# Kernel optimization log

Hardware: AMD Instinct MI355X
Metric: run time of the kernel (lower is better)

The kernel has to match this reference:

```python
import jax, jax.numpy as jnp
import numpy as np

B, T, H, S = 4, 4096, 32, 64   # batch, seq_len, n_head, head_size (n_embd = H*S = 2048)
SCALE = 1.0 / 128.0            # matches wkv(..., scale=1/128) in time_mixing_v5_1


def setup_inputs() -> dict:
    key = jax.random.key(0)
    ks = jax.random.split(key, 5)
    k = jax.random.normal(ks[0], (B, T, H, S), dtype=jnp.float32)
    v = jax.random.normal(ks[1], (B, T, H, S), dtype=jnp.float32)
    r = jax.random.normal(ks[2], (B, T, H, S), dtype=jnp.float32)
    state2 = jnp.zeros((B, H, S, S), dtype=jnp.float32)
    # time_first = exp(w) > 0 in the original; time_decay = exp(-exp(w)) in (0,1)
    time_first = jax.random.uniform(ks[3], (H, S, 1), dtype=jnp.float32, minval=0.1, maxval=1.0)
    time_decay = jax.random.uniform(ks[4], (H, S, 1), dtype=jnp.float32, minval=0.9, maxval=0.999)
    return {"k": k, "v": v, "r": r, "state2": state2,
            "time_first": time_first, "time_decay": time_decay}


def reference(k, v, r, state2, time_first, time_decay):
    """RWKV-5 WKV recurrence (wkv() applied token-by-token via lax.scan).

    Per step (per head):
        s2    = state2 * SCALE
        kv    = k_t (outer) (v_t * SCALE)            # [H,S,S]
        wkv_t = r_t @ (time_first * kv + s2)         # [H,S]
        state2' = (time_decay * s2 + kv) / SCALE
    """
    def scan_one(s0, k_b, v_b, r_b):
        def step(s_raw, inp):
            k_t, v_t, r_t = inp                       # each [H, S]
            s2 = s_raw * SCALE
            kv = jnp.einsum('hs,hd->hsd', k_t, v_t * SCALE)   # outer product per head
            wkv = jnp.einsum('hs,hsd->hd', r_t, time_first * kv + s2)
            s_new = (time_decay * s2 + kv) / SCALE
            return s_new, wkv
        s_final, out = jax.lax.scan(step, s0, (k_b, v_b, r_b))
        return out, s_final                           # out: [T, H, S]

    out, s_final = jax.vmap(scan_one)(state2, k, v, r)
    return out, s_final
```

## Files before the change

kernel.cpp:

```cpp
#include <hip/hip_runtime.h>


namespace {
constexpr int cB = 4, cT = 4096, cH = 32, cS = 64;
constexpr int cTS = cH * cS;
constexpr float cScale = 1.0f / 128.0f;
constexpr int cSC = 8, cSCL = cT / cSC;
constexpr int cL = 64, cNS = cSCL / cL;
constexpr int cBH = cB * cH;
}

typedef float  v2f   __attribute__((ext_vector_type(2)));
typedef __bf16 bf16x8 __attribute__((ext_vector_type(8)));
typedef float  f32x16 __attribute__((ext_vector_type(16)));
typedef unsigned short u16x4 __attribute__((ext_vector_type(4)));
typedef unsigned short u16x8 __attribute__((ext_vector_type(8)));
typedef unsigned int   u32x2 __attribute__((ext_vector_type(2)));
typedef unsigned int   u32x4 __attribute__((ext_vector_type(4)));

#define BARRIER() asm volatile("s_waitcnt lgkmcnt(0)\n\ts_barrier" ::: "memory")

__device__ __forceinline__ float hw_log2(float x) { return __builtin_amdgcn_logf(x); }
__device__ __forceinline__ float hw_exp2(float x) { return __builtin_amdgcn_exp2f(x); }

__device__ __forceinline__ int swzb(int row, int byteInRow) {
    return row * 128 + (byteInRow ^ ((row & 15) << 3));
}
__device__ __forceinline__ int swzbV(int row, int byteInRow) {
    return row * 128 + (byteInRow ^ ((row & 15) << 3) ^ (((row >> 3) & 7) << 4));
}
__device__ __forceinline__ int crow(int r, int hi) {
    return (r & 3) + 8 * (r >> 2) + 4 * hi;
}
__device__ __forceinline__ unsigned short bfb(float x) {
    return __builtin_bit_cast(unsigned short, (__bf16)x);
}
__device__ __forceinline__ bf16x8 ldRowFrag(const unsigned short* T, int row, int col) {
    const char* p = (const char*)T;
    u16x4 a = *(const u16x4*)(p + swzb(row, col * 2));
    u16x4 b = *(const u16x4*)(p + swzb(row, col * 2 + 8));
    u16x8 r = {a[0], a[1], a[2], a[3], b[0], b[1], b[2], b[3]};
    return __builtin_bit_cast(bf16x8, r);
}
__device__ __forceinline__ bf16x8 ldRowFragV(const unsigned short* T, int row, int col) {
    const char* p = (const char*)T;
    u16x4 a = *(const u16x4*)(p + swzbV(row, col * 2));
    u16x4 b = *(const u16x4*)(p + swzbV(row, col * 2 + 8));
    u16x8 r = {a[0], a[1], a[2], a[3], b[0], b[1], b[2], b[3]};
    return __builtin_bit_cast(bf16x8, r);
}
__device__ __forceinline__ bf16x8 ldColFrag(const unsigned short* T, int row0, int col) {
    const char* p = (const char*)T;
    u16x8 r;
#pragma unroll
    for (int e = 0; e < 8; ++e)
        r[e] = *(const unsigned short*)(p + swzb(row0 + e, col * 2));
    return __builtin_bit_cast(bf16x8, r);
}
__device__ __forceinline__ void stRow8(unsigned short* T, int row, int col, u16x8 v) {
    char* p = (char*)T;
    u16x4 a = {v[0], v[1], v[2], v[3]}, b = {v[4], v[5], v[6], v[7]};
    *(u16x4*)(p + swzb(row, col * 2)) = a;
    *(u16x4*)(p + swzb(row, col * 2 + 8)) = b;
}
__device__ __forceinline__ void stElV16(unsigned short* T, int row, int col,
                                        unsigned short v) {
    *(unsigned short*)((char*)T + swzbV(row, col * 2)) = v;
}
__device__ __forceinline__ unsigned cvtpk(float a, float b) {
    unsigned r;
    asm("v_cvt_pk_bf16_f32 %0, %1, %2" : "=v"(r) : "v"(a), "v"(b));
    return r;
}
__device__ __forceinline__ void pack2(const f32x16& m, bf16x8& f0, bf16x8& f1) {
#pragma unroll
    for (int g2 = 0; g2 < 2; ++g2) {
        const int bs = 8 * g2;
        unsigned A0 = cvtpk(m[bs + 0], m[bs + 1]);
        unsigned A1 = cvtpk(m[bs + 2], m[bs + 3]);
        unsigned B0 = cvtpk(m[bs + 4], m[bs + 5]);
        unsigned B1 = cvtpk(m[bs + 6], m[bs + 7]);
        u32x2 r0 = __builtin_amdgcn_permlane32_swap(A0, B0, false, false);
        u32x2 r1 = __builtin_amdgcn_permlane32_swap(A1, B1, false, false);
        u32x4 w = {r0[0], r1[0], r0[1], r1[1]};
        if (g2 == 0) f0 = __builtin_bit_cast(bf16x8, w);
        else         f1 = __builtin_bit_cast(bf16x8, w);
    }
}

__global__ __launch_bounds__(256)
void rwkv5_pass1(const float* __restrict__ K, const float* __restrict__ V,
                 const float* __restrict__ TD, float* __restrict__ Buf) {
    __shared__ alignas(16) unsigned short KWs[2][4096], VSTs[2][4096];
    const int bh = blockIdx.x, sc = blockIdx.y;
    const int b = bh >> 5, h = bh & 31;
    const int tid = threadIdx.x, wid = tid >> 6, l = tid & 63;
    const int lo = l & 31, hi = l >> 5;
    const int dhs = wid >> 1, shs = wid & 1;
    const int dS = lo + 32 * dhs, sS = lo + 32 * shs;
    const size_t tbase = ((size_t)b * cT + (size_t)sc * cSCL) * cTS + h * cS;
    const float *kb = K + tbase, *vb = V + tbase;

    const int st = tid >> 2, c16 = (tid & 3) * 16;
    float ipw[16];
#pragma unroll
    for (int e = 0; e < 16; ++e) {
        const float l2 = hw_log2(TD[h * cS + c16 + e]);
        ipw[e] = hw_exp2(-(float)(st + 1) * l2);
    }
    float tdL = TD[h * cS + sS];
#pragma unroll
    for (int i = 0; i < 6; ++i) tdL *= tdL;

    float kx[16], vx[16];
    auto gload = [&](int cc) {
        const size_t off = ((size_t)(cc * cL + st)) * cTS + c16;
#pragma unroll
        for (int i = 0; i < 4; ++i) {
            *(float4*)&kx[i * 4] = *(const float4*)(kb + off + i * 4);
            *(float4*)&vx[i * 4] = *(const float4*)(vb + off + i * 4);
        }
    };
    auto tileWrite = [&](int bi) {
        const v2f* kx2  = (const v2f*)kx;
        const v2f* vx2  = (const v2f*)vx;
        const v2f* ipw2 = (const v2f*)ipw;
        u16x8 w;
#pragma unroll
        for (int hf = 0; hf < 2; ++hf) {
#pragma unroll
            for (int e2 = 0; e2 < 4; ++e2) {
                v2f m = kx2[hf * 4 + e2] * ipw2[hf * 4 + e2];
                w[2 * e2]     = bfb(m.x);
                w[2 * e2 + 1] = bfb(m.y);
            }
            stRow8(KWs[bi], st, c16 + hf * 8, w);
        }
        const v2f sc2 = {cScale, cScale};
#pragma unroll
        for (int e2 = 0; e2 < 8; ++e2) {
            v2f m = vx2[e2] * sc2;
            stElV16(VSTs[bi], c16 + 2 * e2,     st, bfb(m.x));
            stElV16(VSTs[bi], c16 + 2 * e2 + 1, st, bfb(m.y));
        }
    };

    f32x16 x;
#pragma unroll
    for (int i = 0; i < 16; ++i) x[i] = 0.f;

    gload(0); tileWrite(0); gload(1);
    BARRIER();
#pragma unroll 1
    for (int c = 0; c < cNS; ++c) {
        const int cur = c & 1, nxt = cur ^ 1;
        f32x16 w;
#pragma unroll
        for (int i = 0; i < 16; ++i) w[i] = 0.f;
        __builtin_amdgcn_s_setprio(1);
#pragma unroll
        for (int ks = 0; ks < 4; ++ks) {
            bf16x8 vaf = ldRowFragV(VSTs[cur], dS, ks * 16 + hi * 8);
            bf16x8 kcf = ldColFrag(KWs[cur], ks * 16 + hi * 8, sS);
            w = __builtin_amdgcn_mfma_f32_32x32x16_bf16(vaf, kcf, w, 0, 0, 0);
        }
        __builtin_amdgcn_s_setprio(0);
#pragma unroll
        for (int i = 0; i < 16; ++i) x[i] = tdL * (x[i] + w[i]);
        if (c + 1 < cNS) tileWrite(nxt);
        if (c + 2 < cNS) gload(c + 2);
        BARRIER();
    }
    float* xp = Buf + ((size_t)bh * cSC + sc) * cS * cS;
#pragma unroll
    for (int r = 0; r < 16; ++r)
        xp[(size_t)sS * cS + crow(r, hi) + 32 * dhs] = x[r];
}

__global__ __launch_bounds__(256)
void rwkv5_pass2(const float* __restrict__ S2in, const float* __restrict__ TD,
                 float* __restrict__ Buf) {
    const int bh = blockIdx.x, h = bh & 31;
    const int t = threadIdx.x, s = t >> 2, db = (t & 3) * 16;
    float d = TD[h * cS + s];
#pragma unroll
    for (int i = 0; i < 9; ++i) d *= d;
    float4 x[4];
    const float* s0 = S2in + ((size_t)bh * cS + s) * cS + db;
#pragma unroll
    for (int i = 0; i < 4; ++i) {
        x[i] = *(const float4*)(s0 + i * 4);
        x[i].x *= cScale; x[i].y *= cScale; x[i].z *= cScale; x[i].w *= cScale;
    }
    for (int sc = 0; sc < cSC; ++sc) {
        float* base = Buf + (((size_t)bh * cSC + sc) * cS + s) * cS + db;
        float4 pr[4];
        if (sc < cSC - 1) {
#pragma unroll
            for (int i = 0; i < 4; ++i) pr[i] = *(const float4*)(base + i * 4);
        }
#pragma unroll
        for (int i = 0; i < 4; ++i) *(float4*)(base + i * 4) = x[i];
        if (sc < cSC - 1) {
#pragma unroll
            for (int i = 0; i < 4; ++i) {
                x[i].x = fmaf(d, x[i].x, pr[i].x);
                x[i].y = fmaf(d, x[i].y, pr[i].y);
                x[i].z = fmaf(d, x[i].z, pr[i].z);
                x[i].w = fmaf(d, x[i].w, pr[i].w);
            }
        }
    }
}

__global__ __launch_bounds__(512)
void rwkv5_pass3(const float* __restrict__ K, const float* __restrict__ V,
                 const float* __restrict__ R, const float* __restrict__ TF,
                 const float* __restrict__ TD, const float* __restrict__ Buf,
                 float* __restrict__ Out) {
    __shared__ alignas(16) unsigned short RWs[2][4096], KWs[2][4096],
                                          VSTs[2][4096];
    __shared__ alignas(16) u32x4 XTF[2][2][4][64];
    __shared__ float DIAGs[2][64];
    const int u = blockIdx.x, bh = u >> 3, sc = u & 7;
    const int b = bh >> 5, h = bh & 31;
    const int tid = threadIdx.x, wid = tid >> 6, l = tid & 63;
    const int lo = l & 31, hi = l >> 5;
    const size_t tbase = ((size_t)b * cT + (size_t)sc * cSCL) * cTS + h * cS;
    const float *kb = K + tbase, *vb = V + tbase, *rb = R + tbase;
    float* ob = Out + tbase;

    const int st = tid >> 3, sc8 = (tid & 7) * 8;
    float pwA[8], ipwB[8], tfv[8];
#pragma unroll
    for (int e = 0; e < 8; ++e) {
        const float l2 = hw_log2(TD[h * cS + sc8 + e]);
        pwA[e]  = hw_exp2((float)st * l2);
        ipwB[e] = hw_exp2(-(float)(st + 1) * l2);
        tfv[e]  = TF[h * cS + sc8 + e];
    }
    float kx[8], vx[8], rx[8];
    auto gload = [&](int cc) {
        const size_t off = ((size_t)(cc * cL + st)) * cTS + sc8;
        *(float4*)&kx[0] = *(const float4*)(kb + off);
        *(float4*)&kx[4] = *(const float4*)(kb + off + 4);
        *(float4*)&vx[0] = *(const float4*)(vb + off);
        *(float4*)&vx[4] = *(const float4*)(vb + off + 4);
        *(float4*)&rx[0] = *(const float4*)(rb + off);
        *(float4*)&rx[4] = *(const float4*)(rb + off + 4);
    };
    auto tileWrite = [&](int bi) {
        const v2f* kx2  = (const v2f*)kx;
        const v2f* rx2  = (const v2f*)rx;
        const v2f* vx2  = (const v2f*)vx;
        const v2f* pwA2 = (const v2f*)pwA;
        const v2f* ipw2 = (const v2f*)ipwB;
        const v2f* tf2  = (const v2f*)tfv;
        u16x8 w;
#pragma unroll
        for (int e2 = 0; e2 < 4; ++e2) {
            v2f m = rx2[e2] * pwA2[e2];
            w[2 * e2]     = bfb(m.x);
            w[2 * e2 + 1] = bfb(m.y);
        }
        stRow8(RWs[bi], st, sc8, w);
#pragma unroll
        for (int e2 = 0; e2 < 4; ++e2) {
            v2f m = kx2[e2] * ipw2[e2];
            w[2 * e2]     = bfb(m.x);
            w[2 * e2 + 1] = bfb(m.y);
        }
        stRow8(KWs[bi], st, sc8, w);
        const v2f sc2 = {cScale, cScale};
#pragma unroll
        for (int e2 = 0; e2 < 4; ++e2) {
            v2f m = vx2[e2] * sc2;
            stElV16(VSTs[bi], sc8 + 2 * e2,     st, bfb(m.x));
            stElV16(VSTs[bi], sc8 + 2 * e2 + 1, st, bfb(m.y));
        }
        v2f p2 = {0.f, 0.f};
#pragma unroll
        for (int e2 = 0; e2 < 4; ++e2)
            p2 = (rx2[e2] * kx2[e2]) * tf2[e2] + p2;
        float p = p2.x + p2.y;
        p += __shfl_xor(p, 1, 64);
        p += __shfl_xor(p, 2, 64);
        p += __shfl_xor(p, 4, 64);
        if ((tid & 7) == 0) DIAGs[bi][st] = p;
    };

    const int ih = (wid >> 1) & 1, dh = wid & 1;
    const int shs = (wid >> 1) & 1, dhs = wid & 1;

    f32x16 x;
    float tdLr[16];
    if (wid >= 4) {
        const float* xin = Buf + ((size_t)bh * cSC + sc) * cS * cS;
#pragma unroll
        for (int r = 0; r < 16; ++r) {
            const int s = crow(r, hi) + 32 * shs;
            x[r] = xin[(size_t)s * cS + lo + 32 * dhs];
            float t = TD[h * cS + s];
#pragma unroll
            for (int i = 0; i < 6; ++i) t *= t;
            tdLr[r] = t;
        }
        bf16x8 f0, f1;
        pack2(x, f0, f1);
        XTF[0][dhs][2 * shs][l]     = __builtin_bit_cast(u32x4, f0);
        XTF[0][dhs][2 * shs + 1][l] = __builtin_bit_cast(u32x4, f1);
    }
    gload(0); tileWrite(0); gload(1);
    BARRIER();

#pragma unroll 1
    for (int c = 0; c < cNS; ++c) {
        const int cur = c & 1, nxt = cur ^ 1;
        if (wid < 4) {
            bf16x8 rwf[4];
#pragma unroll
            for (int ks = 0; ks < 4; ++ks)
                rwf[ks] = ldRowFrag(RWs[cur], lo + 32 * ih, ks * 16 + hi * 8);
            bf16x8 af0, af1, af2, af3;
            if (ih == 1) {
                f32x16 aU;
#pragma unroll
                for (int i = 0; i < 16; ++i) aU[i] = 0.f;
                __builtin_amdgcn_s_setprio(1);
#pragma unroll
                for (int ks = 0; ks < 4; ++ks) {
                    bf16x8 kwf = ldRowFrag(KWs[cur], lo, ks * 16 + hi * 8);
                    aU = __builtin_amdgcn_mfma_f32_32x32x16_bf16(kwf, rwf[ks], aU, 0, 0, 0);
                }
                __builtin_amdgcn_s_setprio(0);
                pack2(aU, af0, af1);
            }
            f32x16 aM;
#pragma unroll
            for (int i = 0; i < 16; ++i) aM[i] = 0.f;
            __builtin_amdgcn_s_setprio(1);
#pragma unroll
            for (int ks = 0; ks < 4; ++ks) {
                bf16x8 kwf = ldRowFrag(KWs[cur], lo + 32 * ih, ks * 16 + hi * 8);
                aM = __builtin_amdgcn_mfma_f32_32x32x16_bf16(kwf, rwf[ks], aM, 0, 0, 0);
            }
            __builtin_amdgcn_s_setprio(0);
            const float diagv = DIAGs[cur][lo + 32 * ih];
#pragma unroll
            for (int r = 0; r < 16; ++r) {
                const int cr = crow(r, hi);
                aM[r] = (lo > cr) ? aM[r] : ((lo == cr) ? diagv : 0.f);
            }
            if (ih == 1) pack2(aM, af2, af3);
            else         pack2(aM, af0, af1);
            f32x16 o;
#pragma unroll
            for (int i = 0; i < 16; ++i) o[i] = 0.f;
            __builtin_amdgcn_s_setprio(1);
            o = __builtin_amdgcn_mfma_f32_32x32x16_bf16(
                af0, ldRowFragV(VSTs[cur], lo + 32 * dh, 0 * 16 + hi * 8), o, 0, 0, 0);
            o = __builtin_amdgcn_mfma_f32_32x32x16_bf16(
                af1, ldRowFragV(VSTs[cur], lo + 32 * dh, 1 * 16 + hi * 8), o, 0, 0, 0);
            if (ih == 1) {
                o = __builtin_amdgcn_mfma_f32_32x32x16_bf16(
                    af2, ldRowFragV(VSTs[cur], lo + 32 * dh, 2 * 16 + hi * 8), o, 0, 0, 0);
                o = __builtin_amdgcn_mfma_f32_32x32x16_bf16(
                    af3, ldRowFragV(VSTs[cur], lo + 32 * dh, 3 * 16 + hi * 8), o, 0, 0, 0);
            }
#pragma unroll
            for (int ks = 0; ks < 4; ++ks) {
                bf16x8 xf = __builtin_bit_cast(bf16x8, XTF[cur][dh][ks][l]);
                o = __builtin_amdgcn_mfma_f32_32x32x16_bf16(rwf[ks], xf, o, 0, 0, 0);
            }
            __builtin_amdgcn_s_setprio(0);
            const int t0 = c * cL;
#pragma unroll
            for (int r = 0; r < 16; ++r)
                ob[(size_t)(t0 + crow(r, hi) + 32 * ih) * cTS + 32 * dh + lo] = o[r];
        } else {
            f32x16 w;
#pragma unroll
            for (int i = 0; i < 16; ++i) w[i] = 0.f;
            __builtin_amdgcn_s_setprio(1);
#pragma unroll
            for (int ks = 0; ks < 4; ++ks) {
                bf16x8 kcf = ldColFrag(KWs[cur], ks * 16 + hi * 8, lo + 32 * shs);
                bf16x8 vaf = ldRowFragV(VSTs[cur], lo + 32 * dhs, ks * 16 + hi * 8);
                w = __builtin_amdgcn_mfma_f32_32x32x16_bf16(kcf, vaf, w, 0, 0, 0);
            }
            __builtin_amdgcn_s_setprio(0);
#pragma unroll
            for (int i = 0; i < 16; ++i) x[i] = tdLr[i] * (x[i] + w[i]);
            if (c + 1 < cNS) {
                bf16x8 f0, f1;
                pack2(x, f0, f1);
                XTF[nxt][dhs][2 * shs][l]     = __builtin_bit_cast(u32x4, f0);
                XTF[nxt][dhs][2 * shs + 1][l] = __builtin_bit_cast(u32x4, f1);
            }
        }
        if (c + 1 < cNS) tileWrite(nxt);
        if (c + 2 < cNS) gload(c + 2);
        BARRIER();
    }
    if (wid >= 4 && sc == cSC - 1) {
        float* o2 = Out + (size_t)cB * cT * cTS + (size_t)bh * cS * cS;
#pragma unroll
        for (int r = 0; r < 16; ++r) {
            const int s = crow(r, hi) + 32 * shs;
            o2[(size_t)s * cS + lo + 32 * dhs] = x[r] * 128.0f;
        }
    }
}

extern "C" void kernel_launch(void* const* d_in, const int* in_sizes, int n_in,
                              void* d_out, int out_size, void* d_ws,
                              size_t ws_size, hipStream_t stream) {
    const float* K    = (const float*)d_in[0];
    const float* V    = (const float*)d_in[1];
    const float* R    = (const float*)d_in[2];
    const float* S2in = (const float*)d_in[3];
    const float* TF   = (const float*)d_in[4];
    const float* TD   = (const float*)d_in[5];
    float* OutP = (float*)d_out;
    float* Buf  = (float*)d_ws;
    (void)in_sizes; (void)n_in; (void)ws_size; (void)out_size;

    rwkv5_pass1<<<dim3(cBH, cSC - 1), dim3(256), 0, stream>>>(K, V, TD, Buf);
    rwkv5_pass2<<<dim3(cBH), dim3(256), 0, stream>>>(S2in, TD, Buf);
    rwkv5_pass3<<<dim3(cBH * cSC), dim3(512), 0, stream>>>(K, V, R, TF, TD,
                                                           Buf, OutP);
}
```

Before: 176.1 us.

## Warp-specialize pass1 producers/consumers and fold state prefix scan into pass3

Pass1 now launches 512 threads: four waves only stage K/V tiles into LDS (global load and bf16 conversion) while the other four only run the MFMA chunk-state accumulation, so loads overlap with compute. The separate pass2 kernel that prefix-scanned chunk states is removed. Each pass3 block instead rebuilds its starting state from the initial state plus the preceding chunk sums, weighted by decay^512. This saves a launch and a serialized small kernel, at the cost of redundant prefix work in later-chunk blocks (up to 7 extra 64x64 reads) and an extra S2in read in pass3.

Result: no change. 175.3 us (-0.5%).

```diff
diff --git a/kernel.cpp b/kernel.cpp
--- a/kernel.cpp
+++ b/kernel.cpp
@@ -88,7 +88,7 @@
     }
 }
 
-__global__ __launch_bounds__(256)
+__global__ __launch_bounds__(512)
 void rwkv5_pass1(const float* __restrict__ K, const float* __restrict__ V,
                  const float* __restrict__ TD, float* __restrict__ Buf) {
     __shared__ alignas(16) unsigned short KWs[2][4096], VSTs[2][4096];
@@ -96,21 +96,26 @@
     const int b = bh >> 5, h = bh & 31;
     const int tid = threadIdx.x, wid = tid >> 6, l = tid & 63;
     const int lo = l & 31, hi = l >> 5;
-    const int dhs = wid >> 1, shs = wid & 1;
+    const int dhs = (wid >> 1) & 1, shs = wid & 1;
     const int dS = lo + 32 * dhs, sS = lo + 32 * shs;
+    const int sid = tid - 256;
+    const int st = (sid & 255) >> 2, c16 = (sid & 3) * 16;
     const size_t tbase = ((size_t)b * cT + (size_t)sc * cSCL) * cTS + h * cS;
     const float *kb = K + tbase, *vb = V + tbase;
 
-    const int st = tid >> 2, c16 = (tid & 3) * 16;
     float ipw[16];
-#pragma unroll
-    for (int e = 0; e < 16; ++e) {
-        const float l2 = hw_log2(TD[h * cS + c16 + e]);
-        ipw[e] = hw_exp2(-(float)(st + 1) * l2);
-    }
-    float tdL = TD[h * cS + sS];
-#pragma unroll
-    for (int i = 0; i < 6; ++i) tdL *= tdL;
+    float tdL = 1.0f;
+    if (wid >= 4) {
+#pragma unroll
+        for (int e = 0; e < 16; ++e) {
+            const float l2 = hw_log2(TD[h * cS + c16 + e]);
+            ipw[e] = hw_exp2(-(float)(st + 1) * l2);
+        }
+    } else {
+        tdL = TD[h * cS + sS];
+#pragma unroll
+        for (int i = 0; i < 6; ++i) tdL *= tdL;
+    }
 
     float kx[16], vx[16];
     auto gload = [&](int cc) {
@@ -149,75 +154,44 @@
 #pragma unroll
     for (int i = 0; i < 16; ++i) x[i] = 0.f;
 
-    gload(0); tileWrite(0); gload(1);
+    if (wid >= 4) { gload(0); tileWrite(0); gload(1); }
     BARRIER();
 #pragma unroll 1
     for (int c = 0; c < cNS; ++c) {
         const int cur = c & 1, nxt = cur ^ 1;
-        f32x16 w;
-#pragma unroll
-        for (int i = 0; i < 16; ++i) w[i] = 0.f;
-        __builtin_amdgcn_s_setprio(1);
-#pragma unroll
-        for (int ks = 0; ks < 4; ++ks) {
-            bf16x8 vaf = ldRowFragV(VSTs[cur], dS, ks * 16 + hi * 8);
-            bf16x8 kcf = ldColFrag(KWs[cur], ks * 16 + hi * 8, sS);
-            w = __builtin_amdgcn_mfma_f32_32x32x16_bf16(vaf, kcf, w, 0, 0, 0);
-        }
-        __builtin_amdgcn_s_setprio(0);
-#pragma unroll
-        for (int i = 0; i < 16; ++i) x[i] = tdL * (x[i] + w[i]);
-        if (c + 1 < cNS) tileWrite(nxt);
-        if (c + 2 < cNS) gload(c + 2);
+        if (wid < 4) {
+            f32x16 w;
+#pragma unroll
+            for (int i = 0; i < 16; ++i) w[i] = 0.f;
+            __builtin_amdgcn_s_setprio(1);
+#pragma unroll
+            for (int ks = 0; ks < 4; ++ks) {
+                bf16x8 vaf = ldRowFragV(VSTs[cur], dS, ks * 16 + hi * 8);
+                bf16x8 kcf = ldColFrag(KWs[cur], ks * 16 + hi * 8, sS);
+                w = __builtin_amdgcn_mfma_f32_32x32x16_bf16(vaf, kcf, w, 0, 0, 0);
+            }
+            __builtin_amdgcn_s_setprio(0);
+#pragma unroll
+            for (int i = 0; i < 16; ++i) x[i] = tdL * (x[i] + w[i]);
+        } else {
+            if (c + 1 < cNS) tileWrite(nxt);
+            if (c + 2 < cNS) gload(c + 2);
+        }
         BARRIER();
     }
-    float* xp = Buf + ((size_t)bh * cSC + sc) * cS * cS;
-#pragma unroll
-    for (int r = 0; r < 16; ++r)
-        xp[(size_t)sS * cS + crow(r, hi) + 32 * dhs] = x[r];
-}
-
-__global__ __launch_bounds__(256)
-void rwkv5_pass2(const float* __restrict__ S2in, const float* __restrict__ TD,
-                 float* __restrict__ Buf) {
-    const int bh = blockIdx.x, h = bh & 31;
-    const int t = threadIdx.x, s = t >> 2, db = (t & 3) * 16;
-    float d = TD[h * cS + s];
-#pragma unroll
-    for (int i = 0; i < 9; ++i) d *= d;
-    float4 x[4];
-    const float* s0 = S2in + ((size_t)bh * cS + s) * cS + db;
-#pragma unroll
-    for (int i = 0; i < 4; ++i) {
-        x[i] = *(const float4*)(s0 + i * 4);
-        x[i].x *= cScale; x[i].y *= cScale; x[i].z *= cScale; x[i].w *= cScale;
-    }
-    for (int sc = 0; sc < cSC; ++sc) {
-        float* base = Buf + (((size_t)bh * cSC + sc) * cS + s) * cS + db;
-        float4 pr[4];
-        if (sc < cSC - 1) {
-#pragma unroll
-            for (int i = 0; i < 4; ++i) pr[i] = *(const float4*)(base + i * 4);
-        }
-#pragma unroll
-        for (int i = 0; i < 4; ++i) *(float4*)(base + i * 4) = x[i];
-        if (sc < cSC - 1) {
-#pragma unroll
-            for (int i = 0; i < 4; ++i) {
-                x[i].x = fmaf(d, x[i].x, pr[i].x);
-                x[i].y = fmaf(d, x[i].y, pr[i].y);
-                x[i].z = fmaf(d, x[i].z, pr[i].z);
-                x[i].w = fmaf(d, x[i].w, pr[i].w);
-            }
-        }
+    if (wid < 4) {
+        float* xp = Buf + ((size_t)bh * cSC + sc) * cS * cS;
+#pragma unroll
+        for (int r = 0; r < 16; ++r)
+            xp[(size_t)sS * cS + crow(r, hi) + 32 * dhs] = x[r];
     }
 }
 
 __global__ __launch_bounds__(512)
 void rwkv5_pass3(const float* __restrict__ K, const float* __restrict__ V,
-                 const float* __restrict__ R, const float* __restrict__ TF,
-                 const float* __restrict__ TD, const float* __restrict__ Buf,
-                 float* __restrict__ Out) {
+                 const float* __restrict__ R, const float* __restrict__ S2in,
+                 const float* __restrict__ TF, const float* __restrict__ TD,
+                 const float* __restrict__ Buf, float* __restrict__ Out) {
     __shared__ alignas(16) unsigned short RWs[2][4096], KWs[2][4096],
                                           VSTs[2][4096];
     __shared__ alignas(16) u32x4 XTF[2][2][4][64];
@@ -295,15 +269,27 @@
     f32x16 x;
     float tdLr[16];
     if (wid >= 4) {
-        const float* xin = Buf + ((size_t)bh * cSC + sc) * cS * cS;
+        const float* s2p = S2in + (size_t)bh * cS * cS;
+        float d512[16];
 #pragma unroll
         for (int r = 0; r < 16; ++r) {
             const int s = crow(r, hi) + 32 * shs;
-            x[r] = xin[(size_t)s * cS + lo + 32 * dhs];
             float t = TD[h * cS + s];
 #pragma unroll
             for (int i = 0; i < 6; ++i) t *= t;
             tdLr[r] = t;
+            t *= t; t *= t; t *= t;
+            d512[r] = t;
+            x[r] = s2p[(size_t)s * cS + lo + 32 * dhs] * cScale;
+        }
+#pragma unroll 1
+        for (int j = 0; j < sc; ++j) {
+            const float* pj = Buf + ((size_t)bh * cSC + j) * cS * cS;
+#pragma unroll
+            for (int r = 0; r < 16; ++r) {
+                const int s = crow(r, hi) + 32 * shs;
+                x[r] = fmaf(d512[r], x[r], pj[(size_t)s * cS + lo + 32 * dhs]);
+            }
         }
         bf16x8 f0, f1;
         pack2(x, f0, f1);
@@ -425,8 +411,7 @@
     float* Buf  = (float*)d_ws;
     (void)in_sizes; (void)n_in; (void)ws_size; (void)out_size;
 
-    rwkv5_pass1<<<dim3(cBH, cSC - 1), dim3(256), 0, stream>>>(K, V, TD, Buf);
-    rwkv5_pass2<<<dim3(cBH), dim3(256), 0, stream>>>(S2in, TD, Buf);
-    rwkv5_pass3<<<dim3(cBH * cSC), dim3(512), 0, stream>>>(K, V, R, TF, TD,
-                                                           Buf, OutP);
-}
+    rwkv5_pass1<<<dim3(cBH, cSC - 1), dim3(512), 0, stream>>>(K, V, TD, Buf);
+    rwkv5_pass3<<<dim3(cBH * cSC), dim3(512), 0, stream>>>(K, V, R, S2in, TF,
+                                                           TD, Buf, OutP);
+}
```
